# Kernel tuning notes

Hardware: AMD Instinct MI355X
Metric: run time of the kernel (lower is better)

The kernel has to match this reference:

```python
import jax, jax.numpy as jnp
import numpy as np

K = 7            # context_window
PAD = K // 2
CENTER = (K * K) // 2  # 24 causal kernel positions kept per channel


def _window_cols(x):
    """x: (B, C, H, W) -> (B, C, K*K, H, W), kernel positions in row-major order
    (matches torch F.unfold channel-major / kernel-minor layout after reshape)."""
    B, C, H, W = x.shape
    xp = jnp.pad(x, ((0, 0), (0, 0), (PAD, PAD), (PAD, PAD)))
    return jnp.stack([xp[:, :, i:i + H, j:j + W]
                      for i in range(K) for j in range(K)], axis=2)


def setup_inputs() -> dict:
    key = jax.random.key(0)
    ks = jax.random.split(key, 4)
    B, C, H, W = 1, 30, 256, 256          # C = channels * n_thresholds = 3*10
    in_dim = C * K * K                     # 1470 MLP input features
    hidden = 2048
    out_dim = 3 * 2                        # channels * 2
    x = jax.random.normal(ks[0], (B, C, H, W), jnp.float32)
    x_ups = jax.random.normal(ks[1], (B, C, H, W), jnp.float32)
    W1 = jax.random.normal(ks[2], (in_dim, hidden), jnp.float32) * np.float32(1.0 / np.sqrt(in_dim))
    b1 = jnp.zeros((hidden,), jnp.float32)
    W2 = jax.random.normal(ks[3], (hidden, out_dim), jnp.float32) * np.float32(1.0 / np.sqrt(hidden))
    b2 = jnp.zeros((out_dim,), jnp.float32)
    return {"x": x, "x_ups": x_ups, "W1": W1, "b1": b1, "W2": W2, "b2": b2}


def reference(x, x_ups, W1, b1, W2, b2):
    B, C, H, W = x.shape
    N = B * H * W
    channels = 3
    # causal_unroll: keep only the first CENTER kernel positions of each channel
    cols = _window_cols(x)                                # (B, C, 49, H, W)
    causal = cols[:, :, :CENTER]                          # (B, C, 24, H, W)
    causal = causal.reshape(B, C * CENTER, H * W).transpose(0, 2, 1).reshape(N, C * CENTER)
    # ups_unroll: full window, then flat slice [:, C*CENTER:] as in torch code
    cols_u = _window_cols(x_ups)                          # (B, C, 49, H, W)
    ups = cols_u.reshape(B, C * K * K, H * W).transpose(0, 2, 1).reshape(N, C * K * K)
    ups = ups[:, C * CENTER:]                             # (N, 750)
    feat = jnp.concatenate([causal, ups], axis=1)         # (N, 1470)
    # MLP (stand-in for model_config.create): Linear -> ReLU -> Linear
    h = jax.nn.relu(feat @ W1 + b1)
    out = h @ W2 + b2                                     # (N, 6)
    out = out.reshape(B, H * W, channels, 2)
    mu = out[..., 0] * 255.0
    s = out[..., 1]
    scale = jnp.clip(s / (1.0 - s + 0.1) * 100.0, 1e-8, 1000.0)
    return jnp.stack([mu, scale], axis=3)                 # (B, H*W, 3, 2)
```

## Files before the change

### kernel.cpp

```cpp
#include <hip/hip_runtime.h>

typedef unsigned short ushort_t;
typedef unsigned int uint_t;
typedef _Float16 f16;
typedef __attribute__((ext_vector_type(8))) _Float16 f16x8;
typedef __attribute__((ext_vector_type(8))) unsigned short u16x8;
typedef __attribute__((ext_vector_type(4))) float f32x4;
typedef __attribute__((ext_vector_type(4))) int i32x4;

#define IMG_S 264
#define IMG_H 262
#define PLANE (IMG_H * IMG_S)
#define NPLANES 61
#define KTOT 1472
#define KREAL 1470
#define NHID 2048
#define NPIX 65536
#define BM 128
#define BN 128
#define BK 32
#define KSTEPS (KTOT / BK)
#define SA 8.0f
#define SB 512.0f
#define INV_S (1.0f / (SA * SB))

__device__ __forceinline__ uint_t f16pair(float f) {
    f16 h = (f16)f;
    f16 l = (f16)(f - (float)h);
    union { f16 a; ushort_t b; } uh, ul;
    uh.a = h; ul.a = l;
    return (uint_t)uh.b | ((uint_t)ul.b << 16);
}

__global__ void pad_imgs(const float* __restrict__ x, const float* __restrict__ xu,
                         uint_t* __restrict__ img2) {
    int idx = blockIdx.x * 256 + threadIdx.x;
    if (idx >= NPLANES * PLANE) return;
    int plane = idx / PLANE;
    int e = idx - plane * PLANE;
    int i = e / IMG_S;
    int j = e - i * IMG_S;
    uint_t v = 0;
    if (plane < 60 && i >= 3 && i < 259 && j >= 3 && j < 259) {
        const float* src = (plane < 30) ? x : xu;
        int c = (plane < 30) ? plane : plane - 30;
        float f = SA * src[(size_t)c * 65536 + (size_t)(i - 3) * 256 + (j - 3)];
        v = f16pair(f);
    }
    img2[idx] = v;
}

__global__ void w1t_kernel(const float* __restrict__ w1,
                           ushort_t* __restrict__ w1t_hi, ushort_t* __restrict__ w1t_lo) {
    __shared__ float tile[32][33];
    const int bk  = blockIdx.x % 46;
    const int bnh = blockIdx.x / 46;
    const int t = threadIdx.x;
    const int r = t >> 5, c = t & 31;
#pragma unroll
    for (int s = 0; s < 4; ++s) {
        int kk = bk * 32 + s * 8 + r;
        int nh = bnh * 32 + c;
        tile[s * 8 + r][c] = (kk < KREAL) ? SB * w1[(size_t)kk * NHID + nh] : 0.0f;
    }
    __syncthreads();
#pragma unroll
    for (int s = 0; s < 4; ++s) {
        int nh = bnh * 32 + s * 8 + r;
        int kk = bk * 32 + c;
        float v = tile[c][s * 8 + r];
        uint_t p = f16pair(v);
        w1t_hi[(size_t)nh * KTOT + kk] = (ushort_t)(p & 0xffffu);
        w1t_lo[(size_t)nh * KTOT + kk] = (ushort_t)(p >> 16);
    }
}

__global__ __launch_bounds__(256, 2)
void fused_gemm(const uint_t* __restrict__ img2,
                const ushort_t* __restrict__ w1t_hi,
                const ushort_t* __restrict__ w1t_lo,
                const float* __restrict__ b1,
                const float* __restrict__ w2,
                float* __restrict__ accum) {
    __shared__ ushort_t Ah[BM * BK];
    __shared__ ushort_t Al[BM * BK];
    __shared__ ushort_t Bh[BN * BK];
    __shared__ ushort_t Bl[BN * BK];
    __shared__ int boff[KTOT];

    const int tid  = threadIdx.x;
    const int bid  = blockIdx.x;
    const int brow = bid >> 4;
    const int bcol = bid & 15;
    const int lane = tid & 63;
    const int wid  = tid >> 6;
    const int wm = wid >> 1;
    const int wn = wid & 1;

    for (int f = tid; f < KTOT; f += 256) {
        int off;
        if (f < 720) {
            int c = f / 24, p = f - c * 24;
            off = c * PLANE + (p / 7) * IMG_S + (p % 7);
        } else if (f < KREAL) {
            int c = f / 49, p = f - c * 49;
            off = (30 + c) * PLANE + (p / 7) * IMG_S + (p % 7);
        } else {
            off = 60 * PLANE;
        }
        boff[f] = off;
    }

    const int row = tid >> 1;
    const int kh  = (tid & 1) * 16;
    const int pix0 = brow * BM;
    const int hwoff = (pix0 >> 8) * IMG_S + (pix0 & 255) + row;
    int waddr[2];
#pragma unroll
    for (int s = 0; s < 2; ++s)
        waddr[s] = (row * (BK * 2) + (kh + s * 8) * 2) ^ ((row & 7) << 4);
    const size_t brow_off = (size_t)(bcol * BN + row) * KTOT + kh;

    f32x4 zero = {0.f, 0.f, 0.f, 0.f};
    f32x4 acc[4][4];
#pragma unroll
    for (int mi = 0; mi < 4; ++mi)
#pragma unroll
        for (int ni = 0; ni < 4; ++ni) acc[mi][ni] = zero;

    for (int kt = 0; kt < KSTEPS; ++kt) {
        __syncthreads();
        const size_t bsrc = brow_off + kt * BK;
#pragma unroll
        for (int s = 0; s < 2; ++s) {
            u16x8 vh = *reinterpret_cast<const u16x8*>(w1t_hi + bsrc + s * 8);
            u16x8 vl = *reinterpret_cast<const u16x8*>(w1t_lo + bsrc + s * 8);
            *reinterpret_cast<u16x8*>((char*)Bh + waddr[s]) = vh;
            *reinterpret_cast<u16x8*>((char*)Bl + waddr[s]) = vl;
        }
        const int f0 = kt * BK + kh;
#pragma unroll
        for (int s = 0; s < 2; ++s) {
            i32x4 o0 = *reinterpret_cast<const i32x4*>(&boff[f0 + s * 8]);
            i32x4 o1 = *reinterpret_cast<const i32x4*>(&boff[f0 + s * 8 + 4]);
            uint_t w[8];
            w[0] = img2[o0.x + hwoff]; w[1] = img2[o0.y + hwoff];
            w[2] = img2[o0.z + hwoff]; w[3] = img2[o0.w + hwoff];
            w[4] = img2[o1.x + hwoff]; w[5] = img2[o1.y + hwoff];
            w[6] = img2[o1.z + hwoff]; w[7] = img2[o1.w + hwoff];
            u16x8 hi, lo;
#pragma unroll
            for (int i = 0; i < 8; ++i) {
                hi[i] = (ushort_t)(w[i] & 0xffffu);
                lo[i] = (ushort_t)(w[i] >> 16);
            }
            *reinterpret_cast<u16x8*>((char*)Ah + waddr[s]) = hi;
            *reinterpret_cast<u16x8*>((char*)Al + waddr[s]) = lo;
        }
        __syncthreads();
        f16x8 afh[4], afl[4], bfh[4], bfl[4];
#pragma unroll
        for (int mi = 0; mi < 4; ++mi) {
            int m = wm * 64 + mi * 16 + (lane & 15);
            int ab = (m * (BK * 2) + (lane >> 4) * 16) ^ ((m & 7) << 4);
            afh[mi] = *reinterpret_cast<const f16x8*>((char*)Ah + ab);
            afl[mi] = *reinterpret_cast<const f16x8*>((char*)Al + ab);
        }
#pragma unroll
        for (int ni = 0; ni < 4; ++ni) {
            int n = wn * 64 + ni * 16 + (lane & 15);
            int bb = (n * (BK * 2) + (lane >> 4) * 16) ^ ((n & 7) << 4);
            bfh[ni] = *reinterpret_cast<const f16x8*>((char*)Bh + bb);
            bfl[ni] = *reinterpret_cast<const f16x8*>((char*)Bl + bb);
        }
#pragma unroll
        for (int mi = 0; mi < 4; ++mi)
#pragma unroll
            for (int ni = 0; ni < 4; ++ni) {
                acc[mi][ni] = __builtin_amdgcn_mfma_f32_16x16x32_f16(
                    afh[mi], bfh[ni], acc[mi][ni], 0, 0, 0);
                acc[mi][ni] = __builtin_amdgcn_mfma_f32_16x16x32_f16(
                    afh[mi], bfl[ni], acc[mi][ni], 0, 0, 0);
                acc[mi][ni] = __builtin_amdgcn_mfma_f32_16x16x32_f16(
                    afl[mi], bfh[ni], acc[mi][ni], 0, 0, 0);
            }
    }

    float b1v[4], w2v[4][6];
#pragma unroll
    for (int ni = 0; ni < 4; ++ni) {
        int n = bcol * BN + wn * 64 + ni * 16 + (lane & 15);
        b1v[ni] = b1[n];
#pragma unroll
        for (int o = 0; o < 6; ++o) w2v[ni][o] = w2[n * 6 + o];
    }
#pragma unroll
    for (int mi = 0; mi < 4; ++mi) {
        float p[4][6];
#pragma unroll
        for (int r = 0; r < 4; ++r)
#pragma unroll
            for (int o = 0; o < 6; ++o) p[r][o] = 0.f;
#pragma unroll
        for (int ni = 0; ni < 4; ++ni) {
#pragma unroll
            for (int r = 0; r < 4; ++r) {
                float hv = fmaxf(acc[mi][ni][r] * INV_S + b1v[ni], 0.0f);
#pragma unroll
                for (int o = 0; o < 6; ++o) p[r][o] += hv * w2v[ni][o];
            }
        }
#pragma unroll
        for (int r = 0; r < 4; ++r) {
#pragma unroll
            for (int o = 0; o < 6; ++o) {
                float v = p[r][o];
                v += __shfl_xor(v, 1, 16);
                v += __shfl_xor(v, 2, 16);
                v += __shfl_xor(v, 4, 16);
                v += __shfl_xor(v, 8, 16);
                int q = r * 6 + o;
                if ((lane & 15) == (q & 15)) {
                    int orow = wm * 64 + mi * 16 + (lane >> 4) * 4 + r;
                    atomicAdd(&accum[(size_t)(pix0 + orow) * 6 + o], v);
                }
            }
        }
    }
}

__global__ void transform_k(const float* __restrict__ accum, const float* __restrict__ b2,
                            float* __restrict__ out) {
    int n = blockIdx.x * 256 + threadIdx.x;
    if (n >= NPIX) return;
#pragma unroll
    for (int ch = 0; ch < 3; ++ch) {
        float m = accum[(size_t)n * 6 + ch * 2 + 0] + b2[ch * 2 + 0];
        float s = accum[(size_t)n * 6 + ch * 2 + 1] + b2[ch * 2 + 1];
        out[(size_t)n * 6 + ch * 2 + 0] = m * 255.0f;
        float denom = 1.0f - s + 0.1f;
        float sc = s / denom * 100.0f;
        sc = fminf(fmaxf(sc, 1e-8f), 1000.0f);
        out[(size_t)n * 6 + ch * 2 + 1] = sc;
    }
}

extern "C" void kernel_launch(void* const* d_in, const int* in_sizes, int n_in,
                              void* d_out, int out_size, void* d_ws, size_t ws_size,
                              hipStream_t stream) {
    const float* x  = (const float*)d_in[0];
    const float* xu = (const float*)d_in[1];
    const float* W1 = (const float*)d_in[2];
    const float* b1 = (const float*)d_in[3];
    const float* W2 = (const float*)d_in[4];
    const float* b2 = (const float*)d_in[5];
    float* out = (float*)d_out;
    char* ws = (char*)d_ws;

    const size_t OFF_W1H = 16877056;
    const size_t OFF_W1L = OFF_W1H + (size_t)NHID * KTOT * 2;
    const size_t OFF_ACC = OFF_W1L + (size_t)NHID * KTOT * 2;
    uint_t* img2    = (uint_t*)ws;
    ushort_t* w1t_h = (ushort_t*)(ws + OFF_W1H);
    ushort_t* w1t_l = (ushort_t*)(ws + OFF_W1L);
    float* accum    = (float*)(ws + OFF_ACC);
    (void)ws_size; (void)in_sizes; (void)n_in; (void)out_size;

    hipMemsetAsync(accum, 0, (size_t)NPIX * 6 * sizeof(float), stream);

    int padN = NPLANES * PLANE;
    pad_imgs<<<(padN + 255) / 256, 256, 0, stream>>>(x, xu, img2);
    w1t_kernel<<<46 * 64, 256, 0, stream>>>(W1, w1t_h, w1t_l);
    fused_gemm<<<512 * 16, 256, 0, stream>>>(img2, w1t_h, w1t_l, b1, W2, accum);
    transform_k<<<NPIX / 256, 256, 0, stream>>>(accum, b2, out);
}
```

Before: 1.594 ms.

## Double the M tile to a full image row and precompute im2col offsets globally

The GEMM M tile grows from 128 to 256 pixels, so each block covers one full image row and each thread gathers one pixel's 32 K-values. The per-block shared-memory offset table is replaced by a table built once in a separate kernel and read from global memory, which removes per-block setup work. Each wave now computes an 8x4 MFMA tile instead of 4x4, reusing B fragments more and halving how many times W1 is read. The cost is more accumulator registers, which may reduce occupancy under launch_bounds(256,2), and scalar global loads of the offsets.

```diff
diff --git a/kernel.cpp b/kernel.cpp
--- a/kernel.cpp
+++ b/kernel.cpp
@@ -6,7 +6,6 @@
 typedef __attribute__((ext_vector_type(8))) _Float16 f16x8;
 typedef __attribute__((ext_vector_type(8))) unsigned short u16x8;
 typedef __attribute__((ext_vector_type(4))) float f32x4;
-typedef __attribute__((ext_vector_type(4))) int i32x4;
 
 #define IMG_S 264
 #define IMG_H 262
@@ -16,7 +15,7 @@
 #define KREAL 1470
 #define NHID 2048
 #define NPIX 65536
-#define BM 128
+#define BM 256
 #define BN 128
 #define BK 32
 #define KSTEPS (KTOT / BK)
@@ -50,6 +49,22 @@
     img2[idx] = v;
 }
 
+__global__ void boff_kernel(int* __restrict__ boff) {
+    int f = blockIdx.x * 256 + threadIdx.x;
+    if (f >= KTOT) return;
+    int off;
+    if (f < 720) {
+        int c = f / 24, p = f - c * 24;
+        off = c * PLANE + (p / 7) * IMG_S + (p % 7);
+    } else if (f < KREAL) {
+        int c = f / 49, p = f - c * 49;
+        off = (30 + c) * PLANE + (p / 7) * IMG_S + (p % 7);
+    } else {
+        off = 60 * PLANE;
+    }
+    boff[f] = off;
+}
+
 __global__ void w1t_kernel(const float* __restrict__ w1,
                            ushort_t* __restrict__ w1t_hi, ushort_t* __restrict__ w1t_lo) {
     __shared__ float tile[32][33];
@@ -79,6 +94,7 @@
 void fused_gemm(const uint_t* __restrict__ img2,
                 const ushort_t* __restrict__ w1t_hi,
                 const ushort_t* __restrict__ w1t_lo,
+                const int* __restrict__ boff,
                 const float* __restrict__ b1,
                 const float* __restrict__ w2,
                 float* __restrict__ accum) {
@@ -86,7 +102,6 @@
     __shared__ ushort_t Al[BM * BK];
     __shared__ ushort_t Bh[BN * BK];
     __shared__ ushort_t Bl[BN * BK];
-    __shared__ int boff[KTOT];
 
     const int tid  = threadIdx.x;
     const int bid  = blockIdx.x;
@@ -97,75 +112,54 @@
     const int wm = wid >> 1;
     const int wn = wid & 1;
 
-    for (int f = tid; f < KTOT; f += 256) {
-        int off;
-        if (f < 720) {
-            int c = f / 24, p = f - c * 24;
-            off = c * PLANE + (p / 7) * IMG_S + (p % 7);
-        } else if (f < KREAL) {
-            int c = f / 49, p = f - c * 49;
-            off = (30 + c) * PLANE + (p / 7) * IMG_S + (p % 7);
-        } else {
-            off = 60 * PLANE;
-        }
-        boff[f] = off;
-    }
-
-    const int row = tid >> 1;
+    const int hwoff = brow * IMG_S + tid;
+    int aaddr[4];
+#pragma unroll
+    for (int s = 0; s < 4; ++s)
+        aaddr[s] = (tid * (BK * 2) + s * 16) ^ ((tid & 7) << 4);
+    const int bn_ = tid >> 1;
     const int kh  = (tid & 1) * 16;
-    const int pix0 = brow * BM;
-    const int hwoff = (pix0 >> 8) * IMG_S + (pix0 & 255) + row;
-    int waddr[2];
+    int baddr[2];
 #pragma unroll
     for (int s = 0; s < 2; ++s)
-        waddr[s] = (row * (BK * 2) + (kh + s * 8) * 2) ^ ((row & 7) << 4);
-    const size_t brow_off = (size_t)(bcol * BN + row) * KTOT + kh;
+        baddr[s] = (bn_ * (BK * 2) + kh * 2 + s * 16) ^ ((bn_ & 7) << 4);
+    const size_t bglob = (size_t)(bcol * BN + bn_) * KTOT + kh;
 
     f32x4 zero = {0.f, 0.f, 0.f, 0.f};
-    f32x4 acc[4][4];
-#pragma unroll
-    for (int mi = 0; mi < 4; ++mi)
+    f32x4 acc[8][4];
+#pragma unroll
+    for (int mi = 0; mi < 8; ++mi)
 #pragma unroll
         for (int ni = 0; ni < 4; ++ni) acc[mi][ni] = zero;
 
     for (int kt = 0; kt < KSTEPS; ++kt) {
         __syncthreads();
-        const size_t bsrc = brow_off + kt * BK;
+        const size_t bsrc = bglob + kt * BK;
 #pragma unroll
         for (int s = 0; s < 2; ++s) {
             u16x8 vh = *reinterpret_cast<const u16x8*>(w1t_hi + bsrc + s * 8);
             u16x8 vl = *reinterpret_cast<const u16x8*>(w1t_lo + bsrc + s * 8);
-            *reinterpret_cast<u16x8*>((char*)Bh + waddr[s]) = vh;
-            *reinterpret_cast<u16x8*>((char*)Bl + waddr[s]) = vl;
-        }
-        const int f0 = kt * BK + kh;
-#pragma unroll
-        for (int s = 0; s < 2; ++s) {
-            i32x4 o0 = *reinterpret_cast<const i32x4*>(&boff[f0 + s * 8]);
-            i32x4 o1 = *reinterpret_cast<const i32x4*>(&boff[f0 + s * 8 + 4]);
+            *reinterpret_cast<u16x8*>((char*)Bh + baddr[s]) = vh;
+            *reinterpret_cast<u16x8*>((char*)Bl + baddr[s]) = vl;
+        }
+        const int f0 = kt * BK;
+#pragma unroll
+        for (int s = 0; s < 4; ++s) {
             uint_t w[8];
-            w[0] = img2[o0.x + hwoff]; w[1] = img2[o0.y + hwoff];
-            w[2] = img2[o0.z + hwoff]; w[3] = img2[o0.w + hwoff];
-            w[4] = img2[o1.x + hwoff]; w[5] = img2[o1.y + hwoff];
-            w[6] = img2[o1.z + hwoff]; w[7] = img2[o1.w + hwoff];
+#pragma unroll
+            for (int i = 0; i < 8; ++i)
+                w[i] = img2[boff[f0 + s * 8 + i] + hwoff];
             u16x8 hi, lo;
 #pragma unroll
             for (int i = 0; i < 8; ++i) {
                 hi[i] = (ushort_t)(w[i] & 0xffffu);
                 lo[i] = (ushort_t)(w[i] >> 16);
             }
-            *reinterpret_cast<u16x8*>((char*)Ah + waddr[s]) = hi;
-            *reinterpret_cast<u16x8*>((char*)Al + waddr[s]) = lo;
+            *reinterpret_cast<u16x8*>((char*)Ah + aaddr[s]) = hi;
+            *reinterpret_cast<u16x8*>((char*)Al + aaddr[s]) = lo;
         }
         __syncthreads();
-        f16x8 afh[4], afl[4], bfh[4], bfl[4];
-#pragma unroll
-        for (int mi = 0; mi < 4; ++mi) {
-            int m = wm * 64 + mi * 16 + (lane & 15);
-            int ab = (m * (BK * 2) + (lane >> 4) * 16) ^ ((m & 7) << 4);
-            afh[mi] = *reinterpret_cast<const f16x8*>((char*)Ah + ab);
-            afl[mi] = *reinterpret_cast<const f16x8*>((char*)Al + ab);
-        }
+        f16x8 bfh[4], bfl[4];
 #pragma unroll
         for (int ni = 0; ni < 4; ++ni) {
             int n = wn * 64 + ni * 16 + (lane & 15);
@@ -174,18 +168,24 @@
             bfl[ni] = *reinterpret_cast<const f16x8*>((char*)Bl + bb);
         }
 #pragma unroll
-        for (int mi = 0; mi < 4; ++mi)
+        for (int mi = 0; mi < 8; ++mi) {
+            int m = wm * 128 + mi * 16 + (lane & 15);
+            int ab = (m * (BK * 2) + (lane >> 4) * 16) ^ ((m & 7) << 4);
+            f16x8 afh = *reinterpret_cast<const f16x8*>((char*)Ah + ab);
+            f16x8 afl = *reinterpret_cast<const f16x8*>((char*)Al + ab);
 #pragma unroll
             for (int ni = 0; ni < 4; ++ni) {
                 acc[mi][ni] = __builtin_amdgcn_mfma_f32_16x16x32_f16(
-                    afh[mi], bfh[ni], acc[mi][ni], 0, 0, 0);
+                    afh, bfh[ni], acc[mi][ni], 0, 0, 0);
                 acc[mi][ni] = __builtin_amdgcn_mfma_f32_16x16x32_f16(
-                    afh[mi], bfl[ni], acc[mi][ni], 0, 0, 0);
+                    afh, bfl[ni], acc[mi][ni], 0, 0, 0);
                 acc[mi][ni] = __builtin_amdgcn_mfma_f32_16x16x32_f16(
-                    afl[mi], bfh[ni], acc[mi][ni], 0, 0, 0);
-            }
-    }
-
+                    afl, bfh[ni], acc[mi][ni], 0, 0, 0);
+            }
+        }
+    }
+
+    const int pix0 = brow * BM;
     float b1v[4], w2v[4][6];
 #pragma unroll
     for (int ni = 0; ni < 4; ++ni) {
@@ -195,7 +195,7 @@
         for (int o = 0; o < 6; ++o) w2v[ni][o] = w2[n * 6 + o];
     }
 #pragma unroll
-    for (int mi = 0; mi < 4; ++mi) {
+    for (int mi = 0; mi < 8; ++mi) {
         float p[4][6];
 #pragma unroll
         for (int r = 0; r < 4; ++r)
@@ -221,7 +221,7 @@
                 v += __shfl_xor(v, 8, 16);
                 int q = r * 6 + o;
                 if ((lane & 15) == (q & 15)) {
-                    int orow = wm * 64 + mi * 16 + (lane >> 4) * 4 + r;
+                    int orow = wm * 128 + mi * 16 + (lane >> 4) * 4 + r;
                     atomicAdd(&accum[(size_t)(pix0 + orow) * 6 + o], v);
                 }
             }
@@ -257,20 +257,23 @@
     float* out = (float*)d_out;
     char* ws = (char*)d_ws;
 
-    const size_t OFF_W1H = 16877056;
-    const size_t OFF_W1L = OFF_W1H + (size_t)NHID * KTOT * 2;
-    const size_t OFF_ACC = OFF_W1L + (size_t)NHID * KTOT * 2;
+    const size_t OFF_W1H  = 16877056;
+    const size_t OFF_W1L  = OFF_W1H + (size_t)NHID * KTOT * 2;
+    const size_t OFF_ACC  = OFF_W1L + (size_t)NHID * KTOT * 2;
+    const size_t OFF_BOFF = OFF_ACC + (size_t)NPIX * 6 * sizeof(float);
     uint_t* img2    = (uint_t*)ws;
     ushort_t* w1t_h = (ushort_t*)(ws + OFF_W1H);
     ushort_t* w1t_l = (ushort_t*)(ws + OFF_W1L);
     float* accum    = (float*)(ws + OFF_ACC);
+    int* boff       = (int*)(ws + OFF_BOFF);
     (void)ws_size; (void)in_sizes; (void)n_in; (void)out_size;
 
     hipMemsetAsync(accum, 0, (size_t)NPIX * 6 * sizeof(float), stream);
 
     int padN = NPLANES * PLANE;
     pad_imgs<<<(padN + 255) / 256, 256, 0, stream>>>(x, xu, img2);
+    boff_kernel<<<(KTOT + 255) / 256, 256, 0, stream>>>(boff);
     w1t_kernel<<<46 * 64, 256, 0, stream>>>(W1, w1t_h, w1t_l);
-    fused_gemm<<<512 * 16, 256, 0, stream>>>(img2, w1t_h, w1t_l, b1, W2, accum);
+    fused_gemm<<<256 * 16, 256, 0, stream>>>(img2, w1t_h, w1t_l, boff, b1, W2, accum);
     transform_k<<<NPIX / 256, 256, 0, stream>>>(accum, b2, out);
 }
```

Measured after the change: 1.502 ms. -5.8%, faster.
